# Kernel tuning notes

Measured on AMD Instinct MI355X. Metric: run time of the kernel, lower is better.

Reference implementation:

```python
import jax, jax.numpy as jnp
import numpy as np

L = 2
S = (L + 1) ** 2            # 9 spherical harmonic coefficients
C = 128                     # sphere_channels
H = 128                     # hidden_channels
NH = 8                      # num_heads
A = 32                      # attn_alpha_channels
V = 16                      # attn_value_channels
N = 5000                    # nodes
E = 50000                   # edges
DE = 128                    # invariant edge embedding dim
G = 18                      # S2 grid points

# l of each coefficient in l-major layout [S]
L_OF = np.concatenate([np.full(2 * l + 1, l) for l in range(L + 1)])
IDX_M0 = np.array([l * l + l for l in range(L + 1)])

def _idx_m(m):
    neg = np.array([l * l + l - m for l in range(m, L + 1)])
    pos = np.array([l * l + l + m for l in range(m, L + 1)])
    return neg, pos

IDX_M1_NEG, IDX_M1_POS = _idx_m(1)
IDX_M2_NEG, IDX_M2_POS = _idx_m(2)
# m-major ordering and its inverse permutation back to l-major
PERM = np.concatenate([IDX_M0, IDX_M1_POS, IDX_M1_NEG, IDX_M2_POS, IDX_M2_NEG])
INV_PERM = np.argsort(PERM)


def _silu(x):
    return x * jax.nn.sigmoid(x)


def _layernorm(x, g, b, eps=1e-5):
    mu = x.mean(-1, keepdims=True)
    var = ((x - mu) ** 2).mean(-1, keepdims=True)
    return (x - mu) * jax.lax.rsqrt(var + eps) * g + b


def _smooth_leaky_relu(x, a=0.2):
    return 0.5 * (1 + a) * x + 0.5 * (1 - a) * x * (2 * jax.nn.sigmoid(x) - 1)


def _so2_conv(x, w_m0, b_m0, w_m1, w_m2, cout):
    """SO(2) convolution on rotated embeddings. x: [E,S,Cin] l-major.
    Returns ([E,S,cout] l-major, extra m=0 channels)."""
    e = x.shape[0]
    # m = 0: plain linear over flattened (L+1)*Cin
    x0 = x[:, IDX_M0, :].reshape(e, -1)
    y0 = x0 @ w_m0 + b_m0
    y0_main = y0[:, : (L + 1) * cout].reshape(e, L + 1, cout)
    y0_extra = y0[:, (L + 1) * cout:]
    parts = [y0_main]
    # m > 0: complex (cos/sin) SO2 mixing with shared weight for real/imag
    for neg, pos, w in ((IDX_M1_NEG, IDX_M1_POS, w_m1), (IDX_M2_NEG, IDX_M2_POS, w_m2)):
        nl = len(neg)
        xr = x[:, pos, :].reshape(e, -1)
        xi = x[:, neg, :].reshape(e, -1)
        yr = xr @ w  # [E, 2*nl*cout]
        yi = xi @ w
        yr_r, yr_i = yr[:, : nl * cout], yr[:, nl * cout:]
        yi_r, yi_i = yi[:, : nl * cout], yi[:, nl * cout:]
        parts.append((yr_r - yi_i).reshape(e, nl, cout))   # +m (real)
        parts.append((yr_i + yi_r).reshape(e, nl, cout))   # -m (imag)
    out_m = jnp.concatenate(parts, axis=1)                 # m-major
    return out_m[:, INV_PERM, :], y0_extra


def _s2_act(x, togrid, fromgrid):
    g = jnp.einsum('gs,esc->egc', togrid, x)
    return jnp.einsum('sg,egc->esc', fromgrid, _silu(g))


def _sep_s2_act(scalars, x, togrid, fromgrid):
    t = _s2_act(x, togrid, fromgrid)
    return jnp.concatenate([_silu(scalars)[:, None, :], t[:, 1:, :]], axis=1)


def _so3_linear(x, w, b):
    # w: [L+1, Cin, Cout], shared across m within each l; bias only on l=0
    out = jnp.einsum('nsc,sco->nso', x, w[L_OF])
    return out.at[:, 0, :].add(b)


def _eqv_norm(x, g, b, eps=1e-5):
    # l=0: layernorm over channels; l>0: RMS over (m, channels) per degree
    outs = [_layernorm(x[:, 0:1, :], g[0], b)]
    for l in range(1, L + 1):
        sl = x[:, l * l:(l + 1) * (l + 1), :]
        rms = jnp.sqrt(jnp.mean(sl ** 2, axis=(1, 2), keepdims=True) + eps)
        outs.append(sl / rms * g[l])
    return jnp.concatenate(outs, axis=1)


def _forward(x, edge_distance, wigner, rad_w1, rad_b1, rad_ln_g, rad_ln_b, rad_w2, rad_b2,
             w1_m0, b1_m0, w1_m1, w1_m2, w2_m0, b2_m0, w2_m1, w2_m2,
             alpha_ln_g, alpha_ln_b, alpha_dot, proj_w, proj_b,
             norm1_g, norm1_b, norm2_g, norm2_b,
             gate_w, gate_b, ffn_w1, ffn_b1, ffn_w2, ffn_b2,
             togrid, fromgrid, edge_src, edge_dst):
    # ---------- SO2 equivariant graph attention ----------
    xn = _eqv_norm(x, norm1_g, norm1_b)
    msg = jnp.concatenate([xn[edge_src], xn[edge_dst]], axis=-1)      # [E,S,2C]
    msg = jnp.einsum('eij,ejc->eic', wigner, msg)                     # rotate to edge frame
    # radial function shared across m within each l (use_m_share_rad)
    h = _silu(_layernorm(edge_distance @ rad_w1 + rad_b1, rad_ln_g, rad_ln_b))
    rad = (h @ rad_w2 + rad_b2).reshape(-1, L + 1, 2 * C)             # [E,L+1,2C]
    msg = msg * rad[:, L_OF, :]
    hid, x0_extra = _so2_conv(msg, w1_m0, b1_m0, w1_m1, w1_m2, H)
    x_alpha = x0_extra[:, : NH * A].reshape(-1, NH, A)
    gating = x0_extra[:, NH * A:]                                     # [E,H]
    hid = _sep_s2_act(gating, hid, togrid, fromgrid)
    val, _ = _so2_conv(hid, w2_m0, b2_m0, w2_m1, w2_m2, NH * V)
    val = jnp.einsum('eji,ejc->eic', wigner, val)                     # rotate back (D^T)
    # attention weights with per-destination segment softmax
    a = _smooth_leaky_relu(_layernorm(x_alpha, alpha_ln_g, alpha_ln_b))
    a = jnp.einsum('eha,ha->eh', a, alpha_dot)                        # [E,NH]
    amax = jax.ops.segment_max(a, edge_dst, num_segments=N)
    aexp = jnp.exp(a - amax[edge_dst])
    asum = jax.ops.segment_sum(aexp, edge_dst, num_segments=N)
    attn = aexp / asum[edge_dst]
    msg_out = (val.reshape(-1, S, NH, V) * attn[:, None, :, None]).reshape(-1, S, NH * V)
    node = jax.ops.segment_sum(msg_out, edge_dst, num_segments=N)     # [N,S,NH*V]
    x = x + _so3_linear(node, proj_w, proj_b)
    # ---------- spherical FFN (sep S2 gating) ----------
    xn = _eqv_norm(x, norm2_g, norm2_b)
    gating = xn[:, 0, :] @ gate_w + gate_b
    hh = _so3_linear(xn, ffn_w1, ffn_b1)
    hh = _sep_s2_act(gating, hh, togrid, fromgrid)
    return x + _so3_linear(hh, ffn_w2, ffn_b2)


def setup_inputs() -> dict:
    key = jax.random.key(0)
    ks = iter(jax.random.split(key, 64))
    def nrm(shape, scale=1.0):
        return jax.random.normal(next(ks), shape, dtype=jnp.float32) * scale
    EX = NH * A + H
    inp = {}
    inp['x'] = nrm((N, S, C))
    inp['edge_distance'] = nrm((E, DE))
    inp['wigner'] = nrm((E, S, S), 1.0 / np.sqrt(S))
    inp['rad_w1'] = nrm((DE, 64), 1.0 / np.sqrt(DE)); inp['rad_b1'] = jnp.zeros((64,), jnp.float32)
    inp['rad_ln_g'] = jnp.ones((64,), jnp.float32); inp['rad_ln_b'] = jnp.zeros((64,), jnp.float32)
    inp['rad_w2'] = nrm((64, 2 * C * (L + 1)), 0.05); inp['rad_b2'] = jnp.ones((2 * C * (L + 1),), jnp.float32)
    inp['w1_m0'] = nrm(((L + 1) * 2 * C, (L + 1) * H + EX), 1.0 / np.sqrt((L + 1) * 2 * C))
    inp['b1_m0'] = jnp.zeros(((L + 1) * H + EX,), jnp.float32)
    inp['w1_m1'] = nrm((2 * 2 * C, 2 * 2 * H), 1.0 / np.sqrt(2 * 2 * C))
    inp['w1_m2'] = nrm((2 * C, 2 * H), 1.0 / np.sqrt(2 * C))
    inp['w2_m0'] = nrm(((L + 1) * H, (L + 1) * NH * V), 1.0 / np.sqrt((L + 1) * H))
    inp['b2_m0'] = jnp.zeros(((L + 1) * NH * V,), jnp.float32)
    inp['w2_m1'] = nrm((2 * H, 2 * 2 * NH * V), 1.0 / np.sqrt(2 * H))
    inp['w2_m2'] = nrm((H, 2 * NH * V), 1.0 / np.sqrt(H))
    inp['alpha_ln_g'] = jnp.ones((A,), jnp.float32); inp['alpha_ln_b'] = jnp.zeros((A,), jnp.float32)
    inp['alpha_dot'] = nrm((NH, A), 1.0 / np.sqrt(A))
    inp['proj_w'] = nrm((L + 1, NH * V, C), 1.0 / np.sqrt(NH * V)); inp['proj_b'] = jnp.zeros((C,), jnp.float32)
    inp['norm1_g'] = jnp.ones((L + 1, C), jnp.float32); inp['norm1_b'] = jnp.zeros((C,), jnp.float32)
    inp['norm2_g'] = jnp.ones((L + 1, C), jnp.float32); inp['norm2_b'] = jnp.zeros((C,), jnp.float32)
    inp['gate_w'] = nrm((C, H), 1.0 / np.sqrt(C)); inp['gate_b'] = jnp.zeros((H,), jnp.float32)
    inp['ffn_w1'] = nrm((L + 1, C, H), 1.0 / np.sqrt(C)); inp['ffn_b1'] = jnp.zeros((H,), jnp.float32)
    inp['ffn_w2'] = nrm((L + 1, H, C), 1.0 / np.sqrt(H)); inp['ffn_b2'] = jnp.zeros((C,), jnp.float32)
    inp['togrid'] = nrm((G, S), 1.0 / np.sqrt(S))
    inp['fromgrid'] = nrm((S, G), 1.0 / np.sqrt(G))
    inp['edge_src'] = jax.random.randint(next(ks), (E,), 0, N)
    inp['edge_dst'] = jax.random.randint(next(ks), (E,), 0, N)
    return inp


def reference(x, edge_distance, wigner, rad_w1, rad_b1, rad_ln_g, rad_ln_b, rad_w2, rad_b2,
              w1_m0, b1_m0, w1_m1, w1_m2, w2_m0, b2_m0, w2_m1, w2_m2,
              alpha_ln_g, alpha_ln_b, alpha_dot, proj_w, proj_b,
              norm1_g, norm1_b, norm2_g, norm2_b,
              gate_w, gate_b, ffn_w1, ffn_b1, ffn_w2, ffn_b2,
              togrid, fromgrid, edge_src, edge_dst):
    return _forward(x, edge_distance, wigner, rad_w1, rad_b1, rad_ln_g, rad_ln_b, rad_w2, rad_b2,
                    w1_m0, b1_m0, w1_m1, w1_m2, w2_m0, b2_m0, w2_m1, w2_m2,
                    alpha_ln_g, alpha_ln_b, alpha_dot, proj_w, proj_b,
                    norm1_g, norm1_b, norm2_g, norm2_b,
                    gate_w, gate_b, ffn_w1, ffn_b1, ffn_w2, ffn_b2,
                    togrid, fromgrid, edge_src, edge_dst)
```

## Files before the change

### kernel.cpp

```cpp
#include <hip/hip_runtime.h>
#include <hip/hip_bf16.h>

typedef unsigned short u16;
typedef unsigned int   u32;
typedef __attribute__((ext_vector_type(8))) short short8;
typedef __attribute__((ext_vector_type(4))) float float4v;

#define NN 5000
#define EE 50000

__device__ __forceinline__ float b2f(u16 u){ return __uint_as_float(((u32)u)<<16); }
__device__ __forceinline__ u16 f2b(float f){
  u32 x = __float_as_uint(f);
  u32 r = (x + 0x7fffu + ((x>>16)&1u)) >> 16;
  return (u16)r;
}
__device__ __forceinline__ float ldin(const void* p, size_t i, bool f32){
  return f32 ? ((const float*)p)[i] : b2f(((const u16*)p)[i]);
}
__device__ __forceinline__ float siluf(float x){ return x/(1.f+__expf(-x)); }
__device__ __forceinline__ float waveRedSum(float v){
  #pragma unroll
  for (int m=32;m>=1;m>>=1) v += __shfl_xor(v,m,64);
  return v;
}
__device__ __forceinline__ float red32(float v){
  #pragma unroll
  for (int m=16;m>=1;m>>=1) v += __shfl_xor(v,m,64);
  return v;
}
__device__ __forceinline__ void gload_lds16(const u16* g, u16* l){
  __builtin_amdgcn_global_load_lds((const __attribute__((address_space(1))) void*)g,
                                   (__attribute__((address_space(3))) void*)l, 16, 0, 0);
}


__global__ __launch_bounds__(256) void zero_kernel(float* __restrict__ p, int n){
  for (int i = blockIdx.x*256 + threadIdx.x; i < n; i += gridDim.x*256) p[i] = 0.f;
}

__global__ void detect_kernel(const u32* __restrict__ ng, int* __restrict__ flag){
  if (blockIdx.x == 0 && threadIdx.x == 0) *flag = (ng[0] == 0x3F800000u) ? 1 : 0;
}

__global__ __launch_bounds__(256) void hist_kernel(const int* __restrict__ edst,
    int* __restrict__ counts){
  int e = blockIdx.x*256 + threadIdx.x;
  if (e < EE) atomicAdd(&counts[edst[e]], 1);
}

__global__ __launch_bounds__(1024) void scan_kernel(const int* __restrict__ counts,
    int* __restrict__ row_start, int* __restrict__ cursor){
  __shared__ int buf[1024];
  __shared__ int base;
  const int t = threadIdx.x;
  if (t == 0){ base = 0; row_start[0] = 0; }
  __syncthreads();
  for (int i0 = 0; i0 < NN; i0 += 1024){
    int i = i0 + t;
    int c = (i < NN) ? counts[i] : 0;
    buf[t] = c;
    __syncthreads();
    #pragma unroll
    for (int ofs = 1; ofs < 1024; ofs <<= 1){
      int v = (t >= ofs) ? buf[t-ofs] : 0;
      __syncthreads();
      buf[t] += v;
      __syncthreads();
    }
    if (i < NN){
      int incl = base + buf[t];
      row_start[i+1] = incl;
      cursor[i] = incl - c;
    }
    __syncthreads();
    if (t == 0) base += buf[1023];
    __syncthreads();
  }
}

__global__ __launch_bounds__(256) void place_kernel(const int* __restrict__ edst,
    int* __restrict__ cursor, int* __restrict__ order){
  int e = blockIdx.x*256 + threadIdx.x;
  if (e < EE) order[atomicAdd(&cursor[edst[e]], 1)] = e;
}

__global__ __launch_bounds__(256) void gathercvt_kernel(const int* __restrict__ dflag,
    const void* __restrict__ src, const int* __restrict__ order, int e0,
    u16* __restrict__ dst, int n){
  const bool f32 = (*dflag != 0);
  for (int i = blockIdx.x*256 + threadIdx.x; i < n; i += gridDim.x*256){
    int le = i >> 7, c = i & 127;
    int eg = order[e0 + le];
    dst[i] = f2b(ldin(src, (size_t)eg*128 + c, f32));
  }
}

__device__ __forceinline__ void do_cvtT(bool f32, const void* src, u16* dst,
    int K, int N, int tid, int stride){
  int total = K*N;
  for (int i = tid; i < total; i += stride){
    int n = i / K, k = i - n*K;
    dst[i] = f2b(ldin(src, (size_t)k*N + n, f32));
  }
}
__device__ __forceinline__ void do_cvtT3(bool f32, const void* src, u16* dst,
    int tid, int stride){
  for (int i = tid; i < 49152; i += stride){
    int l = i >> 14, j = i & 16383;
    int n = j >> 7, k = j & 127;
    dst[i] = f2b(ldin(src, (size_t)l*16384 + (size_t)k*128 + n, f32));
  }
}
__device__ __forceinline__ void do_wprepT(bool f32, const void* w, u16* wt,
    int K0, int N0, int tid, int stride){
  int total = 4*N0*K0;
  for (int i = tid; i < total; i += stride){
    int c = i / (2*K0), rr0 = i - c*2*K0;
    float v;
    if (rr0 < K0) v = ldin(w, (size_t)rr0*2*N0 + c, f32);
    else {
      int rr = rr0 - K0;
      if (c < N0) v = -ldin(w, (size_t)rr*2*N0 + N0 + c, f32);
      else        v =  ldin(w, (size_t)rr*2*N0 + (c - N0), f32);
    }
    wt[i] = f2b(v);
  }
}

__global__ __launch_bounds__(256) void prep_all_kernel(const int* __restrict__ dflag,
    const void* w1_m0, const void* w2_m0, const void* rad_w1, const void* rad_w2,
    const void* proj_w, const void* ffn_w1, const void* ffn_w2, const void* gate_w,
    const void* b1, const void* b2, const void* rb1, const void* rb2,
    const void* pb, const void* gb, const void* f1, const void* f2,
    const void* w1_m1, const void* w1_m2, const void* w2_m1, const void* w2_m2,
    const void* togrid, const void* fromgrid,
    u16* w1m0T, u16* w2m0T, u16* rw1T, u16* rw2T,
    u16* projT3, u16* ffn1T3, u16* ffn2T3, u16* gateT,
    u16* b1m0C, u16* b2m0C, u16* rb1C, u16* rb2C,
    u16* pbC, u16* gbC, u16* fb1C, u16* fb2C,
    u16* W1cT, u16* W2cT, u16* W3cT, u16* W4cT,
    float* TGf, float* FGf){
  const bool f32 = (*dflag != 0);
  const int tid = blockIdx.x*256 + threadIdx.x;
  const int stride = gridDim.x*256;
  switch (blockIdx.y){
    case 0:  do_cvtT (f32, w1_m0, w1m0T, 768, 768, tid, stride); break;
    case 1:  do_cvtT (f32, w2_m0, w2m0T, 384, 384, tid, stride); break;
    case 2:  do_cvtT (f32, rad_w1, rw1T, 128, 64,  tid, stride); break;
    case 3:  do_cvtT (f32, rad_w2, rw2T, 64, 768,  tid, stride); break;
    case 4:  do_cvtT3(f32, proj_w, projT3, tid, stride); break;
    case 5:  do_cvtT3(f32, ffn_w1, ffn1T3, tid, stride); break;
    case 6:  do_cvtT3(f32, ffn_w2, ffn2T3, tid, stride); break;
    case 7:  do_cvtT (f32, gate_w, gateT, 128, 128, tid, stride); break;
    case 8:
      if (tid < 768) b1m0C[tid] = f2b(ldin(b1, tid, f32));
      if (tid < 384) b2m0C[tid] = f2b(ldin(b2, tid, f32));
      if (tid < 64)  rb1C[tid]  = f2b(ldin(rb1, tid, f32));
      if (tid < 768) rb2C[tid]  = f2b(ldin(rb2, tid, f32));
      if (tid < 128){
        pbC[tid]  = f2b(ldin(pb, tid, f32));
        gbC[tid]  = f2b(ldin(gb, tid, f32));
        fb1C[tid] = f2b(ldin(f1, tid, f32));
        fb2C[tid] = f2b(ldin(f2, tid, f32));
      }
      break;
    case 9:  do_wprepT(f32, w1_m1, W1cT, 512, 256, tid, stride); break;
    case 10: do_wprepT(f32, w1_m2, W2cT, 256, 128, tid, stride); break;
    case 11: do_wprepT(f32, w2_m1, W3cT, 256, 256, tid, stride); break;
    case 12: do_wprepT(f32, w2_m2, W4cT, 128, 128, tid, stride); break;
    case 13:
      if (tid < 162) TGf[tid] = ldin(togrid, tid, f32);
      else if (tid >= 256 && tid < 418) FGf[tid-256] = ldin(fromgrid, tid-256, f32);
      break;
  }
}

__global__ __launch_bounds__(128) void eqvnorm_kernel(const int* __restrict__ dflag,
    const void* __restrict__ x, int in_always_f32,
    const void* __restrict__ g, const void* __restrict__ b,
    void* __restrict__ out, int out_f32){
  const bool f32 = (*dflag != 0);
  const bool inf32 = in_always_f32 || f32;
  const int n = blockIdx.x, t = threadIdx.x;
  __shared__ float red[2];
  float v[9];
  #pragma unroll
  for (int s=0;s<9;s++) v[s] = ldin(x, (size_t)n*1152 + s*128 + t, inf32);

  auto bsum = [&](float val)->float{
    float w = waveRedSum(val);
    __syncthreads();
    if ((t & 63) == 0) red[t>>6] = w;
    __syncthreads();
    return red[0] + red[1];
  };
  auto store = [&](int idx, float val){
    if (out_f32) ((float*)out)[(size_t)n*1152 + idx] = val;
    else         ((u16*) out)[(size_t)n*1152 + idx] = f2b(val);
  };
  float mu  = bsum(v[0]) * (1.f/128.f);
  float d0  = v[0] - mu;
  float var = bsum(d0*d0) * (1.f/128.f);
  store(t, d0 * rsqrtf(var + 1e-5f) * ldin(g, t, f32) + ldin(b, t, f32));
  float ss1 = v[1]*v[1] + v[2]*v[2] + v[3]*v[3];
  float inv1 = rsqrtf(bsum(ss1)*(1.f/384.f) + 1e-5f);
  float g1 = ldin(g, 128 + t, f32);
  #pragma unroll
  for (int s=1;s<=3;s++) store(s*128 + t, v[s]*inv1*g1);
  float ss2 = 0.f;
  #pragma unroll
  for (int s=4;s<9;s++) ss2 += v[s]*v[s];
  float inv2 = rsqrtf(bsum(ss2)*(1.f/640.f) + 1e-5f);
  float g2 = ldin(g, 256 + t, f32);
  #pragma unroll
  for (int s=4;s<9;s++) store(s*128 + t, v[s]*inv2*g2);
}

__device__ __forceinline__ void gemm_core(u16* AsB, u16* BsB,
    const u16* __restrict__ A, int lda, int K,
    const u16* __restrict__ Wt, int NOUT,
    const u16* __restrict__ bias,
    u16* __restrict__ out0, int ld0, int coloff0, int split,
    u16* __restrict__ out1, int ld1, int M, int r0, int n0){
  const int t = threadIdx.x;
  const int lane = t & 63, wave = t >> 6;
  const int wr = (wave & 1) * 64, wn = (wave >> 1) * 64;
  float4v acc[4][4];
  #pragma unroll
  for (int i=0;i<4;i++)
    #pragma unroll
    for (int j=0;j<4;j++) acc[i][j] = (float4v){0.f,0.f,0.f,0.f};

  const int fr = lane & 15;
  const int fq = (((lane >> 4) ^ ((fr >> 1) & 3)) * 8);

  const int Rw   = wave * 32;
  const int srow = lane >> 2;
  const int scol = (((lane & 3) ^ ((srow >> 1) & 3)) * 8);
  const u16* aG0 = A  + (size_t)(r0 + Rw + srow) * lda + scol;
  const u16* aG1 = aG0 + (size_t)16 * lda;
  const bool aV0 = (r0 + Rw + srow)      < M;
  const bool aV1 = (r0 + Rw + 16 + srow) < M;
  const u16* bG0 = Wt + (size_t)(n0 + Rw + srow) * K + scol;
  const u16* bG1 = bG0 + (size_t)16 * K;
  const bool bV0 = (n0 + Rw + srow)      < NOUT;
  const bool bV1 = (n0 + Rw + 16 + srow) < NOUT;

  auto stage = [&](int buf, int k0){
    u16* lA = AsB + buf*4096 + Rw * 32;
    u16* lB = BsB + buf*4096 + Rw * 32;
    if (aV0) gload_lds16(aG0 + k0, lA);
    if (aV1) gload_lds16(aG1 + k0, lA + 16*32);
    if (bV0) gload_lds16(bG0 + k0, lB);
    if (bV1) gload_lds16(bG1 + k0, lB + 16*32);
  };

  stage(0, 0);
  __syncthreads();
  int cur = 0;
  for (int k0 = 0; k0 < K; k0 += 32){
    const int k1 = k0 + 32;
    if (k1 < K) stage(cur ^ 1, k1);
    short8 af[4], bfv[4];
    #pragma unroll
    for (int i=0;i<4;i++){
      af[i]  = *(const short8*)&AsB[cur*4096 + (wr + i*16 + fr)*32 + fq];
      bfv[i] = *(const short8*)&BsB[cur*4096 + (wn + i*16 + fr)*32 + fq];
    }
    #pragma unroll
    for (int i=0;i<4;i++)
      #pragma unroll
      for (int j=0;j<4;j++)
        acc[i][j] = __builtin_amdgcn_mfma_f32_16x16x32_bf16(af[i], bfv[j], acc[i][j], 0, 0, 0);
    __syncthreads();
    cur ^= 1;
  }
  const int quad = lane >> 4;
  #pragma unroll
  for (int j=0;j<4;j++){
    int col = n0 + wn + j*16 + fr;
    if (col >= NOUT) continue;
    float bv = bias ? b2f(bias[col]) : 0.f;
    #pragma unroll
    for (int i=0;i<4;i++){
      int rbase = r0 + wr + i*16 + quad*4;
      #pragma unroll
      for (int rg=0; rg<4; rg++){
        int row = rbase + rg;
        if (row >= M) continue;
        float v = acc[i][j][rg] + bv;
        if (col < split) out0[(size_t)row*ld0 + coloff0 + col] = f2b(v);
        else             out1[(size_t)row*ld1 + (col - split)] = f2b(v);
      }
    }
  }
}

__device__ __forceinline__ int xcd_swz(int bid, int nwg){
  const int q = nwg >> 3, r = nwg & 7;
  const int xcd = bid & 7, sid = bid >> 3;
  return (xcd < r ? xcd*(q+1) : r*(q+1) + (xcd - r)*q) + sid;
}

__global__ __launch_bounds__(256) void gemm_mfma_kernel(
    const u16* __restrict__ A, int lda, int K,
    const u16* __restrict__ Wt, int NOUT,
    const u16* __restrict__ bias,
    u16* __restrict__ out0, int ld0, int coloff0, int split,
    u16* __restrict__ out1, int ld1, int M){
  __shared__ __align__(16) u16 As[2][128*32];
  __shared__ __align__(16) u16 Bs[2][128*32];
  const int nxg = gridDim.x, nyg = gridDim.y;
  const int bid = blockIdx.y * nxg + blockIdx.x;
  const int swz = xcd_swz(bid, nxg*nyg);
  const int mt = swz / nyg;
  gemm_core(&As[0][0], &Bs[0][0], A, lda, K, Wt, NOUT, bias,
            out0, ld0, coloff0, split, out1, ld1, M, mt*128, (swz - mt*nyg)*128);
}

struct GemmJob {
  const u16* A; const u16* Wt; const u16* bias; u16* out0; u16* out1;
  int lda, K, NOUT, ld0, coloff0, split, ld1;
};
__global__ __launch_bounds__(256) void gemm_mfma3_kernel(
    GemmJob j0, GemmJob j1, GemmJob j2, int ny0, int ny01, int M){
  __shared__ __align__(16) u16 As[2][128*32];
  __shared__ __align__(16) u16 Bs[2][128*32];
  const int nxg = gridDim.x, nyg = gridDim.y;
  const int bid = blockIdx.y * nxg + blockIdx.x;
  const int swz = xcd_swz(bid, nxg*nyg);
  const int mt = swz / nyg;
  const int y  = swz - mt*nyg;
  GemmJob j; int yt;
  if (y < ny0)       { j = j0; yt = y; }
  else if (y < ny01) { j = j1; yt = y - ny0; }
  else               { j = j2; yt = y - ny01; }
  gemm_core(&As[0][0], &Bs[0][0], j.A, j.lda, j.K, j.Wt, j.NOUT, j.bias,
            j.out0, j.ld0, j.coloff0, j.split, j.out1, j.ld1, M, mt*128, yt*128);
}

__global__ __launch_bounds__(256) void gemm_node_kernel(
    const int* __restrict__ dflag,
    const u16* __restrict__ A,
    const u16* __restrict__ W3t,
    const u16* __restrict__ bias,
    const void* __restrict__ resid, int resid_mode,
    void* __restrict__ out, int out_mode,
    const u16* __restrict__ gateW, const u16* __restrict__ gateB,
    u16* __restrict__ gateO){
  const bool f32 = (*dflag != 0);
  int l = blockIdx.y;
  const bool gate = (l >= 3);
  if (gate) l = 0;
  const int rpn  = (l==0) ? 1 : ((l==1) ? 3 : 5);
  const int soff = (l==0) ? 0 : ((l==1) ? 1 : 4);
  const int M = NN * rpn;
  const int r0 = blockIdx.x * 128;
  if (r0 >= M) return;
  __shared__ __align__(16) u16 As[128][40];
  __shared__ __align__(16) u16 Bs[128][40];
  const int t = threadIdx.x;
  const int lane = t & 63, wave = t >> 6;
  const int wr = (wave & 1) * 64, wn = (wave >> 1) * 64;
  float4v acc[4][4];
  #pragma unroll
  for (int i=0;i<4;i++)
    #pragma unroll
    for (int j=0;j<4;j++) acc[i][j] = (float4v){0.f,0.f,0.f,0.f};

  const int sr = t >> 2, sc = (t & 3) * 8;
  const int fr = lane & 15, fq = (lane >> 4) * 8;
  size_t abase[2]; bool aval[2];
  #pragma unroll
  for (int s2=0;s2<2;s2++){
    int m = r0 + sr + s2*64;
    aval[s2] = m < M;
    int n = m / rpn, srow = soff + (m % rpn);
    abase[s2] = (size_t)n*1152 + srow*128 + sc;
  }
  const u16* Wl = gate ? gateW : (W3t + (size_t)l*16384);

  #pragma unroll
  for (int k0 = 0; k0 < 128; k0 += 32){
    #pragma unroll
    for (int s2=0;s2<2;s2++){
      int row = sr + s2*64;
      uint4 av = make_uint4(0u,0u,0u,0u);
      if (aval[s2]) av = *(const uint4*)(A + abase[s2] + k0);
      *(uint4*)&As[row][sc] = av;
      uint4 wv = *(const uint4*)(Wl + (size_t)row*128 + k0 + sc);
      *(uint4*)&Bs[row][sc] = wv;
    }
    __syncthreads();
    short8 af[4], bfr[4];
    #pragma unroll
    for (int i=0;i<4;i++){
      af[i]  = *(const short8*)&As[wr + i*16 + fr][fq];
      bfr[i] = *(const short8*)&Bs[wn + i*16 + fr][fq];
    }
    #pragma unroll
    for (int i=0;i<4;i++)
      #pragma unroll
      for (int j=0;j<4;j++)
        acc[i][j] = __builtin_amdgcn_mfma_f32_16x16x32_bf16(af[i], bfr[j], acc[i][j], 0, 0, 0);
    __syncthreads();
  }
  const int quad = lane >> 4;
  #pragma unroll
  for (int j=0;j<4;j++){
    int col = wn + j*16 + fr;
    float bv;
    if (gate)              bv = b2f(gateB[col]);
    else                   bv = (bias && l==0) ? b2f(bias[col]) : 0.f;
    #pragma unroll
    for (int i=0;i<4;i++){
      int rbase = r0 + wr + i*16 + quad*4;
      #pragma unroll
      for (int rg=0; rg<4; rg++){
        int m = rbase + rg;
        if (m >= M) continue;
        int n = m / rpn, srow = soff + (m % rpn);
        size_t na = (size_t)n*1152 + srow*128 + col;
        float v = acc[i][j][rg] + bv;
        if (gate){ gateO[(size_t)n*128 + col] = f2b(v); continue; }
        if (resid_mode == 1)      v += ((const float*)resid)[na];
        else if (resid_mode == 2) v += ldin(resid, na, f32);
        if (out_mode == 0)       ((u16*)out)[na] = f2b(v);
        else if (out_mode == 1)  ((float*)out)[na] = v;
        else { if (f32) ((float*)out)[na] = v; else ((u16*)out)[na] = f2b(v); }
      }
    }
  }
}

__global__ __launch_bounds__(256) void nodecvt_kernel(const float* __restrict__ node,
    const float* __restrict__ nsum, u16* __restrict__ nodeb){
  for (int i = blockIdx.x*256 + threadIdx.x; i < NN*1152; i += gridDim.x*256){
    int n = i / 1152, c = i & 127, h = c >> 4;
    float ns = nsum[(size_t)n*8 + h];
    float rs = (ns > 0.f) ? 1.f/ns : 0.f;
    nodeb[i] = f2b(node[i] * rs);
  }
}

__global__ __launch_bounds__(128) void node_s2act_kernel(
    const u16* __restrict__ hh, const u16* __restrict__ gating,
    const float* __restrict__ TGf, const float* __restrict__ FGf, u16* __restrict__ hh2){
  const int n = blockIdx.x, t = threadIdx.x;
  float hv[9];
  #pragma unroll
  for (int s=0;s<9;s++) hv[s] = b2f(hh[(size_t)n*1152 + s*128 + t]);
  float gg[18];
  #pragma unroll
  for (int gi=0;gi<18;gi++) gg[gi] = 0.f;
  #pragma unroll
  for (int s=0;s<9;s++){
    float hvs = hv[s];
    #pragma unroll
    for (int gi=0;gi<18;gi++) gg[gi] = fmaf(TGf[gi*9+s], hvs, gg[gi]);
  }
  #pragma unroll
  for (int gi=0;gi<18;gi++) gg[gi] = siluf(gg[gi]);
  hh2[(size_t)n*1152 + t] = f2b(siluf(b2f(gating[(size_t)n*128 + t])));
  #pragma unroll
  for (int s=1;s<9;s++){
    float a = 0.f;
    #pragma unroll
    for (int gi=0;gi<18;gi++) a = fmaf(FGf[s*18+gi], gg[gi], a);
    hh2[(size_t)n*1152 + s*128 + t] = f2b(a);
  }
}

__global__ __launch_bounds__(256) void lnsilu_kernel(const int* __restrict__ dflag,
    u16* __restrict__ H, const void* __restrict__ rlng, const void* __restrict__ rlnb, int M){
  const bool f32 = (*dflag != 0);
  const int r = blockIdx.x*4 + (threadIdx.x >> 6), lane = threadIdx.x & 63;
  if (r >= M) return;
  float h = b2f(H[(size_t)r*64 + lane]);
  float mu = waveRedSum(h) * (1.f/64.f);
  float d = h - mu;
  float var = waveRedSum(d*d) * (1.f/64.f);
  float hn = d * rsqrtf(var + 1e-5f) * ldin(rlng, lane, f32) + ldin(rlnb, lane, f32);
  H[(size_t)r*64 + lane] = f2b(siluf(hn));
}

__global__ __launch_bounds__(256) void edge_rot_kernel(const int* __restrict__ dflag,
    const u16* __restrict__ xn, const void* __restrict__ wig,
    const u16* __restrict__ rad,
    const int* __restrict__ esrc, const int* __restrict__ edst,
    const int* __restrict__ order, int e0, u16* __restrict__ msg){
  const bool f32 = (*dflag != 0);
  const int le = blockIdx.x, t = threadIdx.x;
  const int eg = order[e0 + le];
  __shared__ float W[81];
  if (t < 81) W[t] = ldin(wig, (size_t)eg*81 + t, f32);
  const int src = esrc[eg], dst = edst[eg];
  float pre[9];
  const u16* base = (t < 128) ? (xn + (size_t)src*1152 + t) : (xn + (size_t)dst*1152 + (t-128));
  #pragma unroll
  for (int j=0;j<9;j++) pre[j] = b2f(base[j*128]);
  __syncthreads();
  float rot[9];
  #pragma unroll
  for (int i=0;i<9;i++){
    float a = 0.f;
    #pragma unroll
    for (int j=0;j<9;j++) a = fmaf(W[i*9+j], pre[j], a);
    rot[i] = a;
  }
  float r[3];
  #pragma unroll
  for (int l=0;l<3;l++) r[l] = b2f(rad[(size_t)le*768 + l*256 + t]);
  const int INVP[9] = {0,5,1,3,8,6,2,4,7};
  const int LOF[9]  = {0,1,1,1,2,2,2,2,2};
  u16* mb = msg + (size_t)le*2304 + t;
  #pragma unroll
  for (int i=0;i<9;i++) mb[INVP[i]*256] = f2b(rot[i] * r[LOF[i]]);
}

__global__ __launch_bounds__(256) void s2act_alpha_kernel(const int* __restrict__ dflag,
    const u16* __restrict__ hid, const u16* __restrict__ extra,
    const float* __restrict__ TGf, const float* __restrict__ FGf,
    const void* __restrict__ alng, const void* __restrict__ alnb, const void* __restrict__ adot,
    const int* __restrict__ edst, const int* __restrict__ order, int e0,
    u16* __restrict__ hid2, float* __restrict__ aexp, float* __restrict__ nsum){
  const bool f32 = (*dflag != 0);
  const int le = blockIdx.x, t = threadIdx.x;
  const int p = e0 + le;
  {
    const int h = t >> 5, ai = t & 31;
    float v = b2f(extra[(size_t)le*384 + t]);
    float mu = red32(v) * (1.f/32.f);
    float d = v - mu;
    float var = red32(d*d) * (1.f/32.f);
    float xh = d * rsqrtf(var + 1e-5f) * ldin(alng, ai, f32) + ldin(alnb, ai, f32);
    float sig = 1.f/(1.f + __expf(-xh));
    float sl = 0.6f*xh + 0.4f*xh*(2.f*sig - 1.f);
    float pp = sl * ldin(adot, h*32 + ai, f32);
    float dot = red32(pp);
    if (ai == 0){
      float ex = __expf(dot - 8.f);
      aexp[(size_t)p*8 + h] = ex;
      atomicAdd(&nsum[(size_t)edst[order[p]]*8 + h], ex);
    }
  }
  if (t < 128){
    const int INVP[9] = {0,5,1,3,8,6,2,4,7};
    float hv[9];
    #pragma unroll
    for (int s=0;s<9;s++) hv[s] = b2f(hid[(size_t)le*1152 + INVP[s]*128 + t]);
    float gg[18];
    #pragma unroll
    for (int gi=0;gi<18;gi++) gg[gi] = 0.f;
    #pragma unroll
    for (int s=0;s<9;s++){
      float hvs = hv[s];
      #pragma unroll
      for (int gi=0;gi<18;gi++) gg[gi] = fmaf(TGf[gi*9+s], hvs, gg[gi]);
    }
    #pragma unroll
    for (int gi=0;gi<18;gi++) gg[gi] = siluf(gg[gi]);
    hid2[(size_t)le*1152 + t] = f2b(siluf(b2f(extra[(size_t)le*384 + 256 + t])));
    #pragma unroll
    for (int s=1;s<9;s++){
      float a = 0.f;
      #pragma unroll
      for (int gi=0;gi<18;gi++) a = fmaf(FGf[s*18+gi], gg[gi], a);
      hid2[(size_t)le*1152 + INVP[s]*128 + t] = f2b(a);
    }
  }
}

__global__ __launch_bounds__(128) void unrot_gather_kernel(const int* __restrict__ dflag,
    const u16* __restrict__ val, const void* __restrict__ wig,
    const float* __restrict__ aexp, const int* __restrict__ order,
    const int* __restrict__ row_start, int e0, int Mc, float* __restrict__ node){
  const bool f32 = (*dflag != 0);
  const int n = blockIdx.x, t = threadIdx.x;
  const int s = row_start[n], tend = row_start[n+1];
  int lo = (s > e0) ? s : e0;
  int hi = (tend < e0 + Mc) ? tend : (e0 + Mc);
  if (lo >= hi) return;
  __shared__ float W[81];
  __shared__ float SC[8];
  const int INVP[9] = {0,5,1,3,8,6,2,4,7};
  float acc[9];
  #pragma unroll
  for (int i=0;i<9;i++) acc[i] = 0.f;
  for (int p = lo; p < hi; p++){
    const int le = p - e0;
    const int eg = order[p];
    __syncthreads();
    if (t < 81) W[t] = ldin(wig, (size_t)eg*81 + t, f32);
    if (t >= 120) SC[t-120] = aexp[(size_t)p*8 + (t-120)];
    __syncthreads();
    float vs[9];
    #pragma unroll
    for (int j=0;j<9;j++) vs[j] = b2f(val[(size_t)le*1152 + INVP[j]*128 + t]);
    const float sc = SC[t>>4];
    #pragma unroll
    for (int i=0;i<9;i++){
      float a = 0.f;
      #pragma unroll
      for (int j=0;j<9;j++) a = fmaf(W[j*9+i], vs[j], a);
      acc[i] = fmaf(a, sc, acc[i]);
    }
  }
  const bool full = (s >= e0) && (tend <= e0 + Mc);
  #pragma unroll
  for (int i=0;i<9;i++){
    float* dst = &node[(size_t)n*1152 + i*128 + t];
    if (full) *dst = acc[i];
    else      atomicAdd(dst, acc[i]);
  }
}

extern "C" void kernel_launch(void* const* d_in, const int* in_sizes, int n_in,
                              void* d_out, int out_size, void* d_ws, size_t ws_size,
                              hipStream_t stream){
  (void)in_sizes; (void)n_in; (void)out_size;
  const void* x       = d_in[0];
  const void* edist   = d_in[1];
  const void* wig     = d_in[2];
  const void* rad_w1  = d_in[3];
  const void* rad_b1  = d_in[4];
  const void* rad_lng = d_in[5];
  const void* rad_lnb = d_in[6];
  const void* rad_w2  = d_in[7];
  const void* rad_b2  = d_in[8];
  const void* w1_m0   = d_in[9];
  const void* b1_m0   = d_in[10];
  const void* w1_m1   = d_in[11];
  const void* w1_m2   = d_in[12];
  const void* w2_m0   = d_in[13];
  const void* b2_m0   = d_in[14];
  const void* w2_m1   = d_in[15];
  const void* w2_m2   = d_in[16];
  const void* alng    = d_in[17];
  const void* alnb    = d_in[18];
  const void* adot    = d_in[19];
  const void* proj_w  = d_in[20];
  const void* proj_b  = d_in[21];
  const void* norm1_g = d_in[22];
  const void* norm1_b = d_in[23];
  const void* norm2_g = d_in[24];
  const void* norm2_b = d_in[25];
  const void* gate_w  = d_in[26];
  const void* gate_b  = d_in[27];
  const void* ffn_w1  = d_in[28];
  const void* ffn_b1  = d_in[29];
  const void* ffn_w2  = d_in[30];
  const void* ffn_b2  = d_in[31];
  const void* togrid  = d_in[32];
  const void* fromgrid= d_in[33];
  const int* esrc     = (const int*)d_in[34];
  const int* edst     = (const int*)d_in[35];

  char* wsp = (char*)d_ws;
  size_t off = 0;
  auto alloc = [&](size_t bytes)->char*{
    char* p = wsp + off;
    off = (off + bytes + 255) & ~(size_t)255;
    return p;
  };
  int*  dflag  = (int*) alloc(4);
  u16*  W1cT   = (u16*) alloc((size_t)512*1024*2);
  u16*  W2cT   = (u16*) alloc((size_t)256*512*2);
  u16*  W3cT   = (u16*) alloc((size_t)512*512*2);
  u16*  W4cT   = (u16*) alloc((size_t)256*256*2);
  u16*  w1m0T  = (u16*) alloc((size_t)768*768*2);
  u16*  b1m0C  = (u16*) alloc((size_t)768*2);
  u16*  w2m0T  = (u16*) alloc((size_t)384*384*2);
  u16*  b2m0C  = (u16*) alloc((size_t)384*2);
  u16*  rw1T   = (u16*) alloc((size_t)64*128*2);
  u16*  rb1C   = (u16*) alloc((size_t)64*2);
  u16*  rw2T   = (u16*) alloc((size_t)768*64*2);
  u16*  rb2C   = (u16*) alloc((size_t)768*2);
  u16*  projT3 = (u16*) alloc((size_t)3*16384*2);
  u16*  ffn1T3 = (u16*) alloc((size_t)3*16384*2);
  u16*  ffn2T3 = (u16*) alloc((size_t)3*16384*2);
  u16*  gateT  = (u16*) alloc((size_t)16384*2);
  u16*  pbC    = (u16*) alloc((size_t)128*2);
  u16*  gbC    = (u16*) alloc((size_t)128*2);
  u16*  fb1C   = (u16*) alloc((size_t)128*2);
  u16*  fb2C   = (u16*) alloc((size_t)128*2);
  float* TGf   = (float*)alloc((size_t)162*4);
  float* FGf   = (float*)alloc((size_t)162*4);
  u16*  xn     = (u16*) alloc((size_t)NN*1152*2);
  float* aexp  = (float*)alloc((size_t)EE*8*4);
  float* nsum  = (float*)alloc((size_t)NN*8*4);
  float* node  = (float*)alloc((size_t)NN*1152*4);
  int*  counts = (int*) alloc((size_t)NN*4);
  int*  row_st = (int*) alloc((size_t)(NN+1)*4);
  int*  cursor = (int*) alloc((size_t)NN*4);
  int*  order  = (int*) alloc((size_t)EE*4);
  size_t fixed_end = off;
  size_t avail = (ws_size > fixed_end) ? (ws_size - fixed_end) : 0;

  long long cap = ((long long)avail - 4096) / 7680;
  int Ec;
  if (cap >= 50048) Ec = 50048;
  else {
    long long c128 = cap & ~127LL;
    if (c128 < 128) c128 = 128;
    int nch = (EE + (int)c128 - 1) / (int)c128;
    Ec = ((EE + nch - 1) / nch + 127) & ~127;
  }
  char* cb = wsp + fixed_end;
  u16* msgC   = (u16*)cb;
  u16* hidC   = (u16*)(cb + (size_t)Ec*2304*2);
  u16* extraC = (u16*)(cb + (size_t)Ec*2304*2 + (size_t)Ec*1152*2);
  u16* hid2C  = msgC;
  u16* valC   = hidC;
  u16* edistC = msgC;
  u16* radC   = hidC;
  u16* HrawC  = hidC + (size_t)Ec*768;
  u16*  nodeb  = (u16*)cb;
  float* xnew  = (float*)(cb + (size_t)NN*1152*2);
  u16*  xn2    = (u16*)(cb + (size_t)NN*1152*2 + (size_t)NN*1152*4);
  u16*  gating = xn2 + (size_t)NN*1152;
  u16*  hh     = gating + (size_t)NN*128;
  u16*  hh2    = hh + (size_t)NN*1152;

  detect_kernel<<<1, 64, 0, stream>>>((const u32*)norm1_g, dflag);

  zero_kernel<<<2048, 256, 0, stream>>>(nsum, NN*8 + NN*1152 + NN);

  hist_kernel<<<(EE+255)/256, 256, 0, stream>>>(edst, counts);
  scan_kernel<<<1, 1024, 0, stream>>>(counts, row_st, cursor);
  place_kernel<<<(EE+255)/256, 256, 0, stream>>>(edst, cursor, order);

  prep_all_kernel<<<dim3(256,14), 256, 0, stream>>>(dflag,
      w1_m0, w2_m0, rad_w1, rad_w2, proj_w, ffn_w1, ffn_w2, gate_w,
      b1_m0, b2_m0, rad_b1, rad_b2, proj_b, gate_b, ffn_b1, ffn_b2,
      w1_m1, w1_m2, w2_m1, w2_m2, togrid, fromgrid,
      w1m0T, w2m0T, rw1T, rw2T, projT3, ffn1T3, ffn2T3, gateT,
      b1m0C, b2m0C, rb1C, rb2C, pbC, gbC, fb1C, fb2C,
      W1cT, W2cT, W3cT, W4cT, TGf, FGf);

  eqvnorm_kernel<<<NN, 128, 0, stream>>>(dflag, x, 0, norm1_g, norm1_b, xn, 0);

  for (int e0 = 0; e0 < EE; e0 += Ec){
    int Mc = (EE - e0 < Ec) ? (EE - e0) : Ec;
    int GX = (Mc + 127) / 128;
    gathercvt_kernel<<<dim3((Mc*128+255)/256), 256, 0, stream>>>(dflag, edist, order, e0,
                                                                 edistC, Mc*128);
    gemm_mfma_kernel<<<dim3(GX,1), 256, 0, stream>>>(edistC, 128, 128, rw1T, 64, rb1C,
                                                     HrawC, 64, 0, 64, nullptr, 0, Mc);
    lnsilu_kernel<<<dim3((Mc+3)/4), 256, 0, stream>>>(dflag, HrawC, rad_lng, rad_lnb, Mc);
    gemm_mfma_kernel<<<dim3(GX,6), 256, 0, stream>>>(HrawC, 64, 64, rw2T, 768, rb2C,
                                                     radC, 768, 0, 768, nullptr, 0, Mc);
    edge_rot_kernel<<<Mc, 256, 0, stream>>>(dflag, xn, wig, radC, esrc, edst, order, e0, msgC);
    {
      GemmJob j0{msgC,        w1m0T, b1m0C,   hidC, extraC, 2304, 768,  768, 1152, 0,   384, 384};
      GemmJob j1{msgC + 768,  W1cT,  nullptr, hidC, nullptr,2304, 1024, 512, 1152, 384, 512, 0};
      GemmJob j2{msgC + 1792, W2cT,  nullptr, hidC, nullptr,2304, 512,  256, 1152, 896, 256, 0};
      gemm_mfma3_kernel<<<dim3(GX,12), 256, 0, stream>>>(j0, j1, j2, 6, 10, Mc);
    }
    s2act_alpha_kernel<<<Mc, 256, 0, stream>>>(dflag, hidC, extraC, TGf, FGf, alng,
                                               alnb, adot, edst, order, e0, hid2C, aexp, nsum);
    {
      GemmJob j0{hid2C,       w2m0T, b2m0C,   valC, nullptr, 1152, 384, 384, 1152, 0,   384, 0};
      GemmJob j1{hid2C + 384, W3cT,  nullptr, valC, nullptr, 1152, 512, 512, 1152, 384, 512, 0};
      GemmJob j2{hid2C + 896, W4cT,  nullptr, valC, nullptr, 1152, 256, 256, 1152, 896, 256, 0};
      gemm_mfma3_kernel<<<dim3(GX,9), 256, 0, stream>>>(j0, j1, j2, 3, 7, Mc);
    }
    unrot_gather_kernel<<<NN, 128, 0, stream>>>(dflag, valC, wig, aexp, order, row_st,
                                                e0, Mc, node);
  }

  const int GN2 = (NN*5 + 127)/128;
  nodecvt_kernel<<<2048, 256, 0, stream>>>(node, nsum, nodeb);
  gemm_node_kernel<<<dim3(GN2,3), 256, 0, stream>>>(dflag, nodeb, projT3, pbC,
                                                    x, 2, xnew, 1, nullptr, nullptr, nullptr);
  eqvnorm_kernel<<<NN, 128, 0, stream>>>(dflag, xnew, 1, norm2_g, norm2_b, xn2, 0);
  gemm_node_kernel<<<dim3(GN2,4), 256, 0, stream>>>(dflag, xn2, ffn1T3, fb1C,
                                                    nullptr, 0, hh, 0, gateT, gbC, gating);
  node_s2act_kernel<<<NN, 128, 0, stream>>>(hh, gating, TGf, FGf, hh2);
  gemm_node_kernel<<<dim3(GN2,3), 256, 0, stream>>>(dflag, hh2, ffn2T3, fb2C,
                                                    xnew, 1, d_out, 2, nullptr, nullptr, nullptr);
}
```

Measured before the change: 1.029 ms.

## Pack two edges per block, vectorize bf16 loads, double-buffer Wigner in gather

edge_rot now handles two edges per 256-thread block, with each thread doing two channels through 32-bit packed bf16 loads and stores. s2act_alpha handles two edges per 512-thread block. unrot_gather double-buffers the Wigner matrix and attention scales in shared memory, prefetching the next edge so each iteration needs one barrier instead of two. The aim is to cut block-launch overhead, memory transactions and sync stalls, at the cost of more registers and bounds-guard logic.

```diff
diff --git a/kernel.cpp b/kernel.cpp
--- a/kernel.cpp
+++ b/kernel.cpp
@@ -489,48 +489,72 @@
     const u16* __restrict__ xn, const void* __restrict__ wig,
     const u16* __restrict__ rad,
     const int* __restrict__ esrc, const int* __restrict__ edst,
-    const int* __restrict__ order, int e0, u16* __restrict__ msg){
+    const int* __restrict__ order, int e0, int Mc, u16* __restrict__ msg){
   const bool f32 = (*dflag != 0);
-  const int le = blockIdx.x, t = threadIdx.x;
-  const int eg = order[e0 + le];
-  __shared__ float W[81];
-  if (t < 81) W[t] = ldin(wig, (size_t)eg*81 + t, f32);
+  const int sub = threadIdx.x >> 7;
+  const int tt  = threadIdx.x & 127;
+  const int le  = blockIdx.x*2 + sub;
+  const bool ok = (le < Mc);
+  const int lec = ok ? le : (Mc-1);
+  const int eg  = order[e0 + lec];
+  __shared__ float W[2][81];
+  if (tt < 81) W[sub][tt] = ldin(wig, (size_t)eg*81 + tt, f32);
   const int src = esrc[eg], dst = edst[eg];
-  float pre[9];
-  const u16* base = (t < 128) ? (xn + (size_t)src*1152 + t) : (xn + (size_t)dst*1152 + (t-128));
-  #pragma unroll
-  for (int j=0;j<9;j++) pre[j] = b2f(base[j*128]);
+  const int c0 = 2*tt;
+  const int node = (c0 < 128) ? src : dst;
+  const int f0 = c0 & 127;
+  const u16* base = xn + (size_t)node*1152 + f0;
+  float pre0[9], pre1[9];
+  #pragma unroll
+  for (int j=0;j<9;j++){
+    u32 pk = *(const u32*)(base + j*128);
+    pre0[j] = b2f((u16)(pk & 0xffffu));
+    pre1[j] = b2f((u16)(pk >> 16));
+  }
+  float r0v[3], r1v[3];
+  #pragma unroll
+  for (int l=0;l<3;l++){
+    u32 pk = *(const u32*)(rad + (size_t)lec*768 + l*256 + c0);
+    r0v[l] = b2f((u16)(pk & 0xffffu));
+    r1v[l] = b2f((u16)(pk >> 16));
+  }
   __syncthreads();
-  float rot[9];
-  #pragma unroll
-  for (int i=0;i<9;i++){
-    float a = 0.f;
-    #pragma unroll
-    for (int j=0;j<9;j++) a = fmaf(W[i*9+j], pre[j], a);
-    rot[i] = a;
-  }
-  float r[3];
-  #pragma unroll
-  for (int l=0;l<3;l++) r[l] = b2f(rad[(size_t)le*768 + l*256 + t]);
   const int INVP[9] = {0,5,1,3,8,6,2,4,7};
   const int LOF[9]  = {0,1,1,1,2,2,2,2,2};
-  u16* mb = msg + (size_t)le*2304 + t;
-  #pragma unroll
-  for (int i=0;i<9;i++) mb[INVP[i]*256] = f2b(rot[i] * r[LOF[i]]);
-}
-
-__global__ __launch_bounds__(256) void s2act_alpha_kernel(const int* __restrict__ dflag,
+  u16* mb = msg + (size_t)lec*2304 + c0;
+  #pragma unroll
+  for (int i=0;i<9;i++){
+    float a0 = 0.f, a1 = 0.f;
+    #pragma unroll
+    for (int j=0;j<9;j++){
+      float w = W[sub][i*9+j];
+      a0 = fmaf(w, pre0[j], a0);
+      a1 = fmaf(w, pre1[j], a1);
+    }
+    if (ok){
+      u16 h0 = f2b(a0 * r0v[LOF[i]]);
+      u16 h1 = f2b(a1 * r1v[LOF[i]]);
+      *(u32*)(mb + INVP[i]*256) = (u32)h0 | ((u32)h1 << 16);
+    }
+  }
+}
+
+__global__ __launch_bounds__(512) void s2act_alpha_kernel(const int* __restrict__ dflag,
     const u16* __restrict__ hid, const u16* __restrict__ extra,
     const float* __restrict__ TGf, const float* __restrict__ FGf,
     const void* __restrict__ alng, const void* __restrict__ alnb, const void* __restrict__ adot,
-    const int* __restrict__ edst, const int* __restrict__ order, int e0,
+    const int* __restrict__ edst, const int* __restrict__ order, int e0, int Mc,
     u16* __restrict__ hid2, float* __restrict__ aexp, float* __restrict__ nsum){
   const bool f32 = (*dflag != 0);
-  const int le = blockIdx.x, t = threadIdx.x;
-  const int p = e0 + le;
+  const int sub = threadIdx.x >> 8;
+  const int tt  = threadIdx.x & 255;
+  const int le  = blockIdx.x*2 + sub;
+  const bool ok = (le < Mc);
+  const int lec = ok ? le : (Mc-1);
+  const int p = e0 + lec;
   {
-    const int h = t >> 5, ai = t & 31;
-    float v = b2f(extra[(size_t)le*384 + t]);
+    const int h = tt >> 5, ai = tt & 31;
+    float v = b2f(extra[(size_t)lec*384 + tt]);
     float mu = red32(v) * (1.f/32.f);
     float d = v - mu;
     float var = red32(d*d) * (1.f/32.f);
@@ -539,17 +563,17 @@
     float sl = 0.6f*xh + 0.4f*xh*(2.f*sig - 1.f);
     float pp = sl * ldin(adot, h*32 + ai, f32);
     float dot = red32(pp);
-    if (ai == 0){
+    if (ai == 0 && ok){
       float ex = __expf(dot - 8.f);
       aexp[(size_t)p*8 + h] = ex;
       atomicAdd(&nsum[(size_t)edst[order[p]]*8 + h], ex);
     }
   }
-  if (t < 128){
+  if (tt < 128){
     const int INVP[9] = {0,5,1,3,8,6,2,4,7};
     float hv[9];
     #pragma unroll
-    for (int s=0;s<9;s++) hv[s] = b2f(hid[(size_t)le*1152 + INVP[s]*128 + t]);
+    for (int s=0;s<9;s++) hv[s] = b2f(hid[(size_t)lec*1152 + INVP[s]*128 + tt]);
     float gg[18];
     #pragma unroll
     for (int gi=0;gi<18;gi++) gg[gi] = 0.f;
@@ -561,13 +585,13 @@
     }
     #pragma unroll
     for (int gi=0;gi<18;gi++) gg[gi] = siluf(gg[gi]);
-    hid2[(size_t)le*1152 + t] = f2b(siluf(b2f(extra[(size_t)le*384 + 256 + t])));
+    if (ok) hid2[(size_t)lec*1152 + tt] = f2b(siluf(b2f(extra[(size_t)lec*384 + 256 + tt])));
     #pragma unroll
     for (int s=1;s<9;s++){
       float a = 0.f;
       #pragma unroll
       for (int gi=0;gi<18;gi++) a = fmaf(FGf[s*18+gi], gg[gi], a);
-      hid2[(size_t)le*1152 + INVP[s]*128 + t] = f2b(a);
+      if (ok) hid2[(size_t)lec*1152 + INVP[s]*128 + tt] = f2b(a);
     }
   }
 }
@@ -582,30 +606,39 @@
   int lo = (s > e0) ? s : e0;
   int hi = (tend < e0 + Mc) ? tend : (e0 + Mc);
   if (lo >= hi) return;
-  __shared__ float W[81];
-  __shared__ float SC[8];
+  __shared__ float W[2][81];
+  __shared__ float SC[2][8];
   const int INVP[9] = {0,5,1,3,8,6,2,4,7};
   float acc[9];
   #pragma unroll
   for (int i=0;i<9;i++) acc[i] = 0.f;
+  {
+    const int eg0 = order[lo];
+    if (t < 81) W[0][t] = ldin(wig, (size_t)eg0*81 + t, f32);
+    if (t >= 120) SC[0][t-120] = aexp[(size_t)lo*8 + (t-120)];
+  }
+  __syncthreads();
+  int cur = 0;
   for (int p = lo; p < hi; p++){
+    if (p + 1 < hi){
+      const int eg1 = order[p+1];
+      if (t < 81) W[cur^1][t] = ldin(wig, (size_t)eg1*81 + t, f32);
+      if (t >= 120) SC[cur^1][t-120] = aexp[(size_t)(p+1)*8 + (t-120)];
+    }
     const int le = p - e0;
-    const int eg = order[p];
-    __syncthreads();
-    if (t < 81) W[t] = ldin(wig, (size_t)eg*81 + t, f32);
-    if (t >= 120) SC[t-120] = aexp[(size_t)p*8 + (t-120)];
-    __syncthreads();
     float vs[9];
     #pragma unroll
     for (int j=0;j<9;j++) vs[j] = b2f(val[(size_t)le*1152 + INVP[j]*128 + t]);
-    const float sc = SC[t>>4];
+    const float sc = SC[cur][t>>4];
     #pragma unroll
     for (int i=0;i<9;i++){
       float a = 0.f;
       #pragma unroll
-      for (int j=0;j<9;j++) a = fmaf(W[j*9+i], vs[j], a);
+      for (int j=0;j<9;j++) a = fmaf(W[cur][j*9+i], vs[j], a);
       acc[i] = fmaf(a, sc, acc[i]);
     }
+    __syncthreads();
+    cur ^= 1;
   }
   const bool full = (s >= e0) && (tend <= e0 + Mc);
   #pragma unroll
@@ -751,15 +784,17 @@
     lnsilu_kernel<<<dim3((Mc+3)/4), 256, 0, stream>>>(dflag, HrawC, rad_lng, rad_lnb, Mc);
     gemm_mfma_kernel<<<dim3(GX,6), 256, 0, stream>>>(HrawC, 64, 64, rw2T, 768, rb2C,
                                                      radC, 768, 0, 768, nullptr, 0, Mc);
-    edge_rot_kernel<<<Mc, 256, 0, stream>>>(dflag, xn, wig, radC, esrc, edst, order, e0, msgC);
+    edge_rot_kernel<<<dim3((Mc+1)/2), 256, 0, stream>>>(dflag, xn, wig, radC, esrc, edst,
+                                                        order, e0, Mc, msgC);
     {
       GemmJob j0{msgC,        w1m0T, b1m0C,   hidC, extraC, 2304, 768,  768, 1152, 0,   384, 384};
       GemmJob j1{msgC + 768,  W1cT,  nullptr, hidC, nullptr,2304, 1024, 512, 1152, 384, 512, 0};
       GemmJob j2{msgC + 1792, W2cT,  nullptr, hidC, nullptr,2304, 512,  256, 1152, 896, 256, 0};
       gemm_mfma3_kernel<<<dim3(GX,12), 256, 0, stream>>>(j0, j1, j2, 6, 10, Mc);
     }
-    s2act_alpha_kernel<<<Mc, 256, 0, stream>>>(dflag, hidC, extraC, TGf, FGf, alng,
-                                               alnb, adot, edst, order, e0, hid2C, aexp, nsum);
+    s2act_alpha_kernel<<<dim3((Mc+1)/2), 512, 0, stream>>>(dflag, hidC, extraC, TGf, FGf,
+                                               alng, alnb, adot, edst, order, e0, Mc,
+                                               hid2C, aexp, nsum);
     {
       GemmJob j0{hid2C,       w2m0T, b2m0C,   valC, nullptr, 1152, 384, 384, 1152, 0,   384, 0};
       GemmJob j1{hid2C + 384, W3cT,  nullptr, valC, nullptr, 1152, 512, 512, 1152, 384, 512, 0};
```

After: 1.085 ms. 5.5% more time.
